# Kernel tuning notes

Hardware: AMD Instinct MI355X
Metric: run time of the kernel (lower is better)

## Reference

```python
import jax, jax.numpy as jnp
import numpy as np

# ASPPConv constants (from init_kwargs)
K = 9                      # kernel_size
DILATION = 6
PAD = DILATION * (K // 2)  # 24, 'same' padding for dilated conv
SIGMA = DILATION * 1.0     # self.sigma = dilation * sigma
BN_EPS = 1e-5


def setup_inputs() -> dict:
    key = jax.random.key(0)
    k1, k2, k3 = jax.random.split(key, 3)
    B, C, O, L = 8, 256, 16384, 0  # placeholder to keep names readable
    B, Cin, Cout, L = 8, 256, 256, 16384
    x = jax.random.normal(k1, (B, Cin, L), dtype=jnp.float32)
    coords = jax.random.uniform(k2, (B, 3, L), dtype=jnp.float32)  # xyz per point
    weight = jax.random.normal(k3, (Cout, Cin, K), dtype=jnp.float32) * 0.05
    gamma = jnp.ones((Cout,), jnp.float32)
    beta = jnp.zeros((Cout,), jnp.float32)
    return {"x": x, "coords": coords, "weight": weight, "gamma": gamma, "beta": beta}


def _weighted_conv1d(x, coords, weight):
    """Dilated conv1d where each tap is scaled by a Gaussian of the squared
    euclidean distance between the tap's coordinates and the center point's
    coordinates: w_k = exp(-||c_k - c_center||^2 / (2*sigma^2)).
    Zero padding (matches F.unfold) for both x and coords."""
    B, C, L = x.shape
    x_pad = jnp.pad(x, ((0, 0), (0, 0), (PAD, PAD)))
    c_pad = jnp.pad(coords, ((0, 0), (0, 0), (PAD, PAD)))
    inv_2s2 = 1.0 / (2.0 * SIGMA * SIGMA)
    out = jnp.zeros((B, weight.shape[0], L), x.dtype)
    # K=9 taps: small fixed loop; avoids materializing the [B,C,K,L] unfold.
    for k in range(K):
        off = k * DILATION
        xk = jax.lax.dynamic_slice_in_dim(x_pad, off, L, axis=2)   # [B,C,L]
        ck = jax.lax.dynamic_slice_in_dim(c_pad, off, L, axis=2)   # [B,3,L]
        dist2 = jnp.sum((ck - coords) ** 2, axis=1)                # [B,L]
        wk = jnp.exp(-dist2 * inv_2s2)                             # [B,L]
        out = out + jnp.einsum('bcl,oc->bol', xk * wk[:, None, :], weight[:, :, k])
    return out


def reference(x, coords, weight, gamma, beta):
    y = _weighted_conv1d(x, coords, weight)                        # [B,O,L]
    # BatchNorm1d (training mode): stats over batch and length per channel
    mean = jnp.mean(y, axis=(0, 2), keepdims=True)
    var = jnp.var(y, axis=(0, 2), keepdims=True)
    y = (y - mean) * jax.lax.rsqrt(var + BN_EPS)
    y = y * gamma[None, :, None] + beta[None, :, None]
    return jax.nn.relu(y)
```

## Files before the change

### kernel.cpp

```cpp
#include <hip/hip_runtime.h>
#include <hip/hip_bf16.h>

#define LEN   16384
#define CIN   256
#define COUT  256
#define NB    8
#define NTAP  9
#define DIL   6
#define PADW  24
#define NSTEP 72
#define PADROWS (LEN + 2*PADW)

typedef __bf16 bf16x8 __attribute__((ext_vector_type(8)));
typedef float  f32x4  __attribute__((ext_vector_type(4)));
typedef unsigned short u16;
typedef u16 u16x8 __attribute__((ext_vector_type(8)));

#define WKT_BYTES  (NB*NTAP*LEN*4)
#define WB_BYTES   (NSTEP*256*32*2)
#define XT_OFF     (WKT_BYTES + WB_BYTES)
#define XT_BYTES   ((size_t)NB*PADROWS*256*2)
#define SUMS_OFF   (XT_OFF + XT_BYTES)
#define SCB_OFF    (SUMS_OFF + 512*4)

#define GLOAD_LDS(g, l) __builtin_amdgcn_global_load_lds( \
    (const __attribute__((address_space(1))) void*)(g),   \
    (__attribute__((address_space(3))) void*)(l), 16, 0, 0)

__device__ __forceinline__ u16 f2bf(float v) {
    unsigned u = __builtin_bit_cast(unsigned, v);
    u += 0x7FFFu + ((u >> 16) & 1u);
    return (u16)(u >> 16);
}

__global__ __launch_bounds__(256) void k_wk(const float* __restrict__ coords,
                                            float* __restrict__ wkt) {
    int i = blockIdx.x * 256 + threadIdx.x;
    if (i >= NB * NTAP * LEN) return;
    int l = i & (LEN - 1);
    int bk = i >> 14;
    int k = bk % NTAP, b = bk / NTAP;
    const float* cb = coords + (size_t)b * 3 * LEN;
    int lt = l + k * DIL - PADW;
    bool ok = (unsigned)lt < (unsigned)LEN;
    float d2 = 0.f;
#pragma unroll
    for (int j = 0; j < 3; ++j) {
        float cc = cb[j * LEN + l];
        float ct = ok ? cb[j * LEN + lt] : 0.f;
        float d = ct - cc;
        d2 += d * d;
    }
    wkt[i] = expf(-d2 * (1.f / 72.f));
}

__global__ __launch_bounds__(256) void k_wb(const float* __restrict__ W,
                                            u16* __restrict__ Wb) {
    int i = blockIdx.x * 256 + threadIdx.x;
    if (i >= NSTEP * 256 * 32) return;
    int j = i & 31;
    int o = (i >> 5) & 255;
    int s = i >> 13;
    int tap   = s % 9;
    int chunk = s / 9;
    int c = chunk * 32 + j;
    Wb[i] = f2bf(W[((size_t)o * CIN + c) * NTAP + tap]);
}

__global__ __launch_bounds__(256) void k_xt(const float* __restrict__ x,
                                            u16* __restrict__ xt) {
    __shared__ float t[64 * 65];
    const int tid = threadIdx.x;
    const int cg  = blockIdx.x;
    const int rg  = blockIdx.y;
    const int b   = blockIdx.z;
    const int lx0 = rg * 64 - PADW;
#pragma unroll
    for (int i = 0; i < 4; ++i) {
        int c  = i * 16 + (tid >> 4);
        int l4 = (tid & 15) * 4;
        int lx = lx0 + l4;
        f32x4 v = {};
        if (lx >= 0 && lx + 3 < LEN)
            v = *reinterpret_cast<const f32x4*>(
                x + ((size_t)b * CIN + cg * 64 + c) * LEN + lx);
        float* tr = &t[c * 65 + l4];
        tr[0] = v[0]; tr[1] = v[1]; tr[2] = v[2]; tr[3] = v[3];
    }
    __syncthreads();
#pragma unroll
    for (int m = 0; m < 2; ++m) {
        int l    = m * 32 + (tid >> 3);
        int c0   = (tid & 7) * 8;
        int prow = rg * 64 + l;
        if (prow < PADROWS) {
            u16x8 o;
#pragma unroll
            for (int j = 0; j < 8; ++j) o[j] = f2bf(t[(c0 + j) * 65 + l]);
            *reinterpret_cast<u16x8*>(
                xt + ((size_t)b * PADROWS + prow) * 256 + cg * 64 + c0) = o;
        }
    }
}

__global__ __launch_bounds__(256, 3) void k_conv(
    const u16*   __restrict__ xt,
    const float* __restrict__ wkt,
    const u16*   __restrict__ Wb,
    float* __restrict__ y,
    float* __restrict__ sums)
{
    const int lt = blockIdx.x;
    const int ob = blockIdx.y;
    const int b  = blockIdx.z;
    const int l0 = lt * 128;
    const int tid  = threadIdx.x;
    const int lane = tid & 63;
    const int wid  = tid >> 6;
    const int wr = wid >> 1;
    const int wc = wid & 1;

    __shared__ u16 As[3][4096];
    __shared__ u16 Bs[3][4096];
    __shared__ float wkl[NTAP * 128];

    for (int i = tid; i < NTAP * 128; i += 256) {
        int k = i >> 7, l = i & 127;
        wkl[i] = wkt[((size_t)b * NTAP + k) * LEN + l0 + l];
    }

    f32x4 acc[4][4] = {};

    const u16* wbBase = Wb + (size_t)ob * 4096;
    const u16* xtBase = xt + (size_t)b * PADROWS * 256;
    const int srcswz = ((lane & 3) ^ ((lane >> 3) & 3)) * 8;
    const int rsub   = lane >> 2;

    auto stage = [&](int slot, int tap, int chunk) {
        const int s = chunk * 9 + tap;
#pragma unroll
        for (int j = 0; j < 2; ++j) {
            const int q = wid * 2 + j;
            const u16* ga = wbBase + (size_t)s * 8192 + (q * 16 + rsub) * 32 + srcswz;
            GLOAD_LDS(ga, &As[slot][q * 512]);
            const u16* gb = xtBase
                + (size_t)(l0 + q * 16 + rsub + 6 * tap) * 256
                + chunk * 32 + srcswz;
            GLOAD_LDS(gb, &Bs[slot][q * 512]);
        }
    };

    const int fr    = lane & 15;
    const int rdoff = fr * 32 + (((lane >> 4) ^ ((fr >> 1) & 3)) * 8);
    const int col   = lane & 15;
    const int rg    = lane >> 4;

    stage(0, 0, 0);
    stage(1, 1, 0);

    int rslot = 0, wslot = 2;
    int tap = 0, chunk = 0;
    int st = 2, sc = 0;
    const f32x4 zf = {};

    for (int s = 0; s < NSTEP; ++s) {
        if (s < NSTEP - 1) asm volatile("s_waitcnt vmcnt(4) lgkmcnt(0)" ::: "memory");
        else               asm volatile("s_waitcnt vmcnt(0) lgkmcnt(0)" ::: "memory");
        asm volatile("s_barrier" ::: "memory");
        if (s + 2 < NSTEP) {
            stage(wslot, st, sc);
            if (++st == NTAP) { st = 0; ++sc; }
        }

        bf16x8 afr[4], bfr[4];
        const u16* Ab = &As[rslot][wr * 2048 + rdoff];
        const u16* Bb = &Bs[rslot][wc * 2048 + rdoff];
#pragma unroll
        for (int mi = 0; mi < 4; ++mi)
            afr[mi] = *reinterpret_cast<const bf16x8*>(Ab + mi * 512);
#pragma unroll
        for (int ni = 0; ni < 4; ++ni)
            bfr[ni] = *reinterpret_cast<const bf16x8*>(Bb + ni * 512);

        float wv[4];
#pragma unroll
        for (int ni = 0; ni < 4; ++ni)
            wv[ni] = wkl[tap * 128 + wc * 64 + ni * 16 + col];

        __builtin_amdgcn_s_setprio(1);
#pragma unroll
        for (int mi = 0; mi < 4; ++mi) {
            f32x4 t0 = __builtin_amdgcn_mfma_f32_16x16x32_bf16(afr[mi], bfr[0], zf, 0, 0, 0);
            f32x4 t1 = __builtin_amdgcn_mfma_f32_16x16x32_bf16(afr[mi], bfr[1], zf, 0, 0, 0);
            f32x4 t2 = __builtin_amdgcn_mfma_f32_16x16x32_bf16(afr[mi], bfr[2], zf, 0, 0, 0);
            f32x4 t3 = __builtin_amdgcn_mfma_f32_16x16x32_bf16(afr[mi], bfr[3], zf, 0, 0, 0);
#pragma unroll
            for (int r = 0; r < 4; ++r) {
                acc[mi][0][r] += wv[0] * t0[r];
                acc[mi][1][r] += wv[1] * t1[r];
                acc[mi][2][r] += wv[2] * t2[r];
                acc[mi][3][r] += wv[3] * t3[r];
            }
        }
        __builtin_amdgcn_s_setprio(0);

        if (++tap == NTAP) { tap = 0; ++chunk; }
        rslot = (rslot == 2) ? 0 : rslot + 1;
        wslot = (wslot == 2) ? 0 : wslot + 1;
    }

    float* yb = y + ((size_t)b * COUT + ob * 128 + wr * 64) * LEN + l0 + wc * 64;
#pragma unroll
    for (int mi = 0; mi < 4; ++mi) {
#pragma unroll
        for (int r = 0; r < 4; ++r) {
            const int o_loc = mi * 16 + rg * 4 + r;
            float s1 = 0.f, s2 = 0.f;
#pragma unroll
            for (int ni = 0; ni < 4; ++ni) {
                float v = acc[mi][ni][r];
                yb[(size_t)o_loc * LEN + ni * 16 + col] = v;
                s1 += v;
                s2 += v * v;
            }
#pragma unroll
            for (int m = 1; m < 16; m <<= 1) {
                s1 += __shfl_xor(s1, m, 64);
                s2 += __shfl_xor(s2, m, 64);
            }
            if (col == 0) {
                int o = ob * 128 + wr * 64 + o_loc;
                atomicAdd(&sums[o], s1);
                atomicAdd(&sums[COUT + o], s2);
            }
        }
    }
}

__global__ __launch_bounds__(256) void k_stats(const float* __restrict__ sums,
                                               const float* __restrict__ gamma,
                                               const float* __restrict__ beta,
                                               float* __restrict__ scb) {
    int o = threadIdx.x;
    const float inv_n = 1.f / (float)(NB * LEN);
    float mean = sums[o] * inv_n;
    float var  = sums[COUT + o] * inv_n - mean * mean;
    float sc = gamma[o] * rsqrtf(var + 1e-5f);
    scb[o]        = sc;
    scb[COUT + o] = beta[o] - mean * sc;
}

__global__ __launch_bounds__(256) void k_norm(float* __restrict__ y,
                                              const float* __restrict__ scb) {
    const int total4 = NB * COUT * LEN / 4;
    int i = blockIdx.x * 256 + threadIdx.x;
    for (; i < total4; i += gridDim.x * 256) {
        f32x4 v = reinterpret_cast<f32x4*>(y)[i];
        int o = (i >> 12) & 255;
        float sc = scb[o], bi = scb[COUT + o];
#pragma unroll
        for (int j = 0; j < 4; ++j)
            v[j] = fmaxf(v[j] * sc + bi, 0.f);
        reinterpret_cast<f32x4*>(y)[i] = v;
    }
}

extern "C" void kernel_launch(void* const* d_in, const int* in_sizes, int n_in,
                              void* d_out, int out_size, void* d_ws, size_t ws_size,
                              hipStream_t stream) {
    const float* x      = (const float*)d_in[0];
    const float* coords = (const float*)d_in[1];
    const float* W      = (const float*)d_in[2];
    const float* gamma  = (const float*)d_in[3];
    const float* beta   = (const float*)d_in[4];
    float* out = (float*)d_out;
    char*  ws  = (char*)d_ws;

    float* wkt  = (float*)ws;
    u16*   Wb   = (u16*)(ws + WKT_BYTES);
    u16*   xtp  = (u16*)(ws + XT_OFF);
    float* sums = (float*)(ws + SUMS_OFF);
    float* scb  = (float*)(ws + SCB_OFF);

    hipMemsetAsync(sums, 0, 512 * 4, stream);

    k_wk<<<(NB * NTAP * LEN + 255) / 256, 256, 0, stream>>>(coords, wkt);
    k_wb<<<(NSTEP * 256 * 32 + 255) / 256, 256, 0, stream>>>(W, Wb);
    k_xt<<<dim3(4, (PADROWS + 63) / 64, NB), 256, 0, stream>>>(x, xtp);

    dim3 g(LEN / 128, 2, NB);
    k_conv<<<g, 256, 0, stream>>>(xtp, wkt, Wb, out, sums);

    k_stats<<<1, 256, 0, stream>>>(sums, gamma, beta, scb);
    k_norm<<<2048, 256, 0, stream>>>(out, scb);
}
```

Baseline: 449.9 us.

## Fold Gaussian tap weights into B tile via register staging, accumulate MFMA directly

```diff
diff --git a/kernel.cpp b/kernel.cpp
--- a/kernel.cpp
+++ b/kernel.cpp
@@ -122,93 +122,122 @@
 
     __shared__ u16 As[3][4096];
     __shared__ u16 Bs[3][4096];
-    __shared__ float wkl[NTAP * 128];
-
-    for (int i = tid; i < NTAP * 128; i += 256) {
-        int k = i >> 7, l = i & 127;
-        wkl[i] = wkt[((size_t)b * NTAP + k) * LEN + l0 + l];
-    }
 
     f32x4 acc[4][4] = {};
 
-    const u16* wbBase = Wb + (size_t)ob * 4096;
-    const u16* xtBase = xt + (size_t)b * PADROWS * 256;
+    const u16*   wbBase = Wb + (size_t)ob * 4096;
+    const u16*   xtBase = xt + (size_t)b * PADROWS * 256;
+    const float* wkBase = wkt + (size_t)b * NTAP * LEN;
+
     const int srcswz = ((lane & 3) ^ ((lane >> 3) & 3)) * 8;
     const int rsub   = lane >> 2;
-
-    auto stage = [&](int slot, int tap, int chunk) {
-        const int s = chunk * 9 + tap;
+    auto stageA = [&](int slot, int s) {
 #pragma unroll
         for (int j = 0; j < 2; ++j) {
             const int q = wid * 2 + j;
-            const u16* ga = wbBase + (size_t)s * 8192 + (q * 16 + rsub) * 32 + srcswz;
-            GLOAD_LDS(ga, &As[slot][q * 512]);
-            const u16* gb = xtBase
-                + (size_t)(l0 + q * 16 + rsub + 6 * tap) * 256
-                + chunk * 32 + srcswz;
-            GLOAD_LDS(gb, &Bs[slot][q * 512]);
+            GLOAD_LDS(wbBase + (size_t)s * 8192 + (q * 16 + rsub) * 32 + srcswz,
+                      &As[slot][q * 512]);
         }
     };
 
+    const int brow = tid >> 1;
+    const int bh   = tid & 1;
+    const int bsw  = (brow >> 1) & 3;
+    const int bwr  = brow * 32 + (((bh * 2) ^ bsw) * 8);
+
+    auto gloadB = [&](u16x8& v0, u16x8& v1, float& w, int tap, int chunk) {
+        const u16* gp = xtBase + (size_t)(l0 + brow + 6 * tap) * 256
+                        + chunk * 32 + bh * 16;
+        v0 = *reinterpret_cast<const u16x8*>(gp);
+        v1 = *reinterpret_cast<const u16x8*>(gp + 8);
+        w  = wkBase[(size_t)tap * LEN + l0 + brow];
+    };
+    auto writeB = [&](int slot, u16x8 v0, u16x8 v1, float w) {
+        u16x8 o0, o1;
+#pragma unroll
+        for (int j = 0; j < 8; ++j) {
+            float f0 = __builtin_bit_cast(float, ((unsigned)v0[j]) << 16) * w;
+            float f1 = __builtin_bit_cast(float, ((unsigned)v1[j]) << 16) * w;
+            o0[j] = f2bf(f0);
+            o1[j] = f2bf(f1);
+        }
+        *reinterpret_cast<u16x8*>(&Bs[slot][bwr])     = o0;
+        *reinterpret_cast<u16x8*>(&Bs[slot][bwr ^ 8]) = o1;
+    };
+
     const int fr    = lane & 15;
-    const int rdoff = fr * 32 + (((lane >> 4) ^ ((fr >> 1) & 3)) * 8);
-    const int col   = lane & 15;
-    const int rg    = lane >> 4;
-
-    stage(0, 0, 0);
-    stage(1, 1, 0);
-
-    int rslot = 0, wslot = 2;
-    int tap = 0, chunk = 0;
-    int st = 2, sc = 0;
-    const f32x4 zf = {};
-
-    for (int s = 0; s < NSTEP; ++s) {
-        if (s < NSTEP - 1) asm volatile("s_waitcnt vmcnt(4) lgkmcnt(0)" ::: "memory");
-        else               asm volatile("s_waitcnt vmcnt(0) lgkmcnt(0)" ::: "memory");
-        asm volatile("s_barrier" ::: "memory");
-        if (s + 2 < NSTEP) {
-            stage(wslot, st, sc);
-            if (++st == NTAP) { st = 0; ++sc; }
-        }
-
-        bf16x8 afr[4], bfr[4];
-        const u16* Ab = &As[rslot][wr * 2048 + rdoff];
-        const u16* Bb = &Bs[rslot][wc * 2048 + rdoff];
+    const int kg    = lane >> 4;
+    const int rdoff = fr * 32 + ((kg ^ ((fr >> 1) & 3)) * 8);
+    bf16x8 afr[4], bfr[4];
+    auto readFrags = [&](int slot) {
+        const u16* Ab = &As[slot][wr * 2048 + rdoff];
+        const u16* Bb = &Bs[slot][wc * 2048 + rdoff];
 #pragma unroll
         for (int mi = 0; mi < 4; ++mi)
             afr[mi] = *reinterpret_cast<const bf16x8*>(Ab + mi * 512);
 #pragma unroll
         for (int ni = 0; ni < 4; ++ni)
             bfr[ni] = *reinterpret_cast<const bf16x8*>(Bb + ni * 512);
-
-        float wv[4];
-#pragma unroll
-        for (int ni = 0; ni < 4; ++ni)
-            wv[ni] = wkl[tap * 128 + wc * 64 + ni * 16 + col];
-
+    };
+    auto domfma = [&]() {
         __builtin_amdgcn_s_setprio(1);
 #pragma unroll
-        for (int mi = 0; mi < 4; ++mi) {
-            f32x4 t0 = __builtin_amdgcn_mfma_f32_16x16x32_bf16(afr[mi], bfr[0], zf, 0, 0, 0);
-            f32x4 t1 = __builtin_amdgcn_mfma_f32_16x16x32_bf16(afr[mi], bfr[1], zf, 0, 0, 0);
-            f32x4 t2 = __builtin_amdgcn_mfma_f32_16x16x32_bf16(afr[mi], bfr[2], zf, 0, 0, 0);
-            f32x4 t3 = __builtin_amdgcn_mfma_f32_16x16x32_bf16(afr[mi], bfr[3], zf, 0, 0, 0);
-#pragma unroll
-            for (int r = 0; r < 4; ++r) {
-                acc[mi][0][r] += wv[0] * t0[r];
-                acc[mi][1][r] += wv[1] * t1[r];
-                acc[mi][2][r] += wv[2] * t2[r];
-                acc[mi][3][r] += wv[3] * t3[r];
-            }
-        }
+        for (int mi = 0; mi < 4; ++mi)
+#pragma unroll
+            for (int ni = 0; ni < 4; ++ni)
+                acc[mi][ni] = __builtin_amdgcn_mfma_f32_16x16x32_bf16(
+                    afr[mi], bfr[ni], acc[mi][ni], 0, 0, 0);
         __builtin_amdgcn_s_setprio(0);
-
-        if (++tap == NTAP) { tap = 0; ++chunk; }
-        rslot = (rslot == 2) ? 0 : rslot + 1;
-        wslot = (wslot == 2) ? 0 : wslot + 1;
-    }
-
+    };
+
+    u16x8 vE0, vE1, vO0, vO1;
+    float wE, wO;
+    stageA(0, 0);
+    gloadB(vE0, vE1, wE, 0, 0);
+    __builtin_amdgcn_sched_barrier(0);
+    stageA(1, 1);
+    gloadB(vO0, vO1, wO, 1, 0);
+    asm volatile("s_waitcnt vmcnt(5)" ::: "memory");
+    writeB(0, vE0, vE1, wE);
+    asm volatile("s_waitcnt lgkmcnt(0)" ::: "memory");
+    asm volatile("s_barrier" ::: "memory");
+
+    int sl0 = 0, sl1 = 1, sl2 = 2;
+    int st = 2, sc = 0;
+
+    for (int t = 0; t < 35; ++t) {
+        stageA(sl2, 2 * t + 2);
+        gloadB(vE0, vE1, wE, st, sc);
+        if (++st == NTAP) { st = 0; ++sc; }
+        readFrags(sl0);
+        asm volatile("s_waitcnt vmcnt(5)" ::: "memory");
+        writeB(sl1, vO0, vO1, wO);
+        asm volatile("s_waitcnt lgkmcnt(0)" ::: "memory");
+        asm volatile("s_barrier" ::: "memory");
+        domfma();
+        stageA(sl0, 2 * t + 3);
+        gloadB(vO0, vO1, wO, st, sc);
+        if (++st == NTAP) { st = 0; ++sc; }
+        readFrags(sl1);
+        asm volatile("s_waitcnt vmcnt(5)" ::: "memory");
+        writeB(sl2, vE0, vE1, wE);
+        asm volatile("s_waitcnt lgkmcnt(0)" ::: "memory");
+        asm volatile("s_barrier" ::: "memory");
+        domfma();
+        int tmp = sl2; sl2 = sl1; sl1 = sl0; sl0 = tmp;
+    }
+
+    readFrags(sl0);
+    asm volatile("s_waitcnt vmcnt(0)" ::: "memory");
+    writeB(sl1, vO0, vO1, wO);
+    asm volatile("s_waitcnt lgkmcnt(0)" ::: "memory");
+    asm volatile("s_barrier" ::: "memory");
+    domfma();
+    readFrags(sl1);
+    domfma();
+
+    const int col = lane & 15;
+    const int rg  = lane >> 4;
     float* yb = y + ((size_t)b * COUT + ob * 128 + wr * 64) * LEN + l0 + wc * 64;
 #pragma unroll
     for (int mi = 0; mi < 4; ++mi) {
```

Result: faster. 426.0 us (-5.3%).

## Switch conv GEMM to fp16 and fold tap weights into B operand

Applied to the files above, without the earlier changes.

```diff
diff --git a/kernel.cpp b/kernel.cpp
--- a/kernel.cpp
+++ b/kernel.cpp
@@ -11,7 +11,7 @@
 #define NSTEP 72
 #define PADROWS (LEN + 2*PADW)
 
-typedef __bf16 bf16x8 __attribute__((ext_vector_type(8)));
+typedef _Float16 f16x8 __attribute__((ext_vector_type(8)));
 typedef float  f32x4  __attribute__((ext_vector_type(4)));
 typedef unsigned short u16;
 typedef u16 u16x8 __attribute__((ext_vector_type(8)));
@@ -27,10 +27,9 @@
     (const __attribute__((address_space(1))) void*)(g),   \
     (__attribute__((address_space(3))) void*)(l), 16, 0, 0)
 
-__device__ __forceinline__ u16 f2bf(float v) {
-    unsigned u = __builtin_bit_cast(unsigned, v);
-    u += 0x7FFFu + ((u >> 16) & 1u);
-    return (u16)(u >> 16);
+__device__ __forceinline__ u16 f2h(float v) {
+    _Float16 h = (_Float16)v;
+    return __builtin_bit_cast(u16, h);
 }
 
 __global__ __launch_bounds__(256) void k_wk(const float* __restrict__ coords,
@@ -64,7 +63,7 @@
     int tap   = s % 9;
     int chunk = s / 9;
     int c = chunk * 32 + j;
-    Wb[i] = f2bf(W[((size_t)o * CIN + c) * NTAP + tap]);
+    Wb[i] = f2h(W[((size_t)o * CIN + c) * NTAP + tap]);
 }
 
 __global__ __launch_bounds__(256) void k_xt(const float* __restrict__ x,
@@ -96,7 +95,7 @@
         if (prow < PADROWS) {
             u16x8 o;
 #pragma unroll
-            for (int j = 0; j < 8; ++j) o[j] = f2bf(t[(c0 + j) * 65 + l]);
+            for (int j = 0; j < 8; ++j) o[j] = f2h(t[(c0 + j) * 65 + l]);
             *reinterpret_cast<u16x8*>(
                 xt + ((size_t)b * PADROWS + prow) * 256 + cg * 64 + c0) = o;
         }
@@ -122,11 +121,11 @@
 
     __shared__ u16 As[3][4096];
     __shared__ u16 Bs[3][4096];
-    __shared__ float wkl[NTAP * 128];
+    __shared__ _Float16 wkl16[NTAP * 128];
 
     for (int i = tid; i < NTAP * 128; i += 256) {
         int k = i >> 7, l = i & 127;
-        wkl[i] = wkt[((size_t)b * NTAP + k) * LEN + l0 + l];
+        wkl16[i] = (_Float16)wkt[((size_t)b * NTAP + k) * LEN + l0 + l];
     }
 
     f32x4 acc[4][4] = {};
@@ -161,7 +160,6 @@
     int rslot = 0, wslot = 2;
     int tap = 0, chunk = 0;
     int st = 2, sc = 0;
-    const f32x4 zf = {};
 
     for (int s = 0; s < NSTEP; ++s) {
         if (s < NSTEP - 1) asm volatile("s_waitcnt vmcnt(4) lgkmcnt(0)" ::: "memory");
@@ -172,36 +170,29 @@
             if (++st == NTAP) { st = 0; ++sc; }
         }
 
-        bf16x8 afr[4], bfr[4];
+        f16x8 afr[4], bs[4];
         const u16* Ab = &As[rslot][wr * 2048 + rdoff];
         const u16* Bb = &Bs[rslot][wc * 2048 + rdoff];
 #pragma unroll
         for (int mi = 0; mi < 4; ++mi)
-            afr[mi] = *reinterpret_cast<const bf16x8*>(Ab + mi * 512);
-#pragma unroll
-        for (int ni = 0; ni < 4; ++ni)
-            bfr[ni] = *reinterpret_cast<const bf16x8*>(Bb + ni * 512);
-
-        float wv[4];
-#pragma unroll
-        for (int ni = 0; ni < 4; ++ni)
-            wv[ni] = wkl[tap * 128 + wc * 64 + ni * 16 + col];
+            afr[mi] = *reinterpret_cast<const f16x8*>(Ab + mi * 512);
+#pragma unroll
+        for (int ni = 0; ni < 4; ++ni) {
+            f16x8 bf = *reinterpret_cast<const f16x8*>(Bb + ni * 512);
+            _Float16 w = wkl16[tap * 128 + wc * 64 + ni * 16 + col];
+            f16x8 w8;
+#pragma unroll
+            for (int j = 0; j < 8; ++j) w8[j] = w;
+            bs[ni] = bf * w8;
+        }
 
         __builtin_amdgcn_s_setprio(1);
 #pragma unroll
-        for (int mi = 0; mi < 4; ++mi) {
-            f32x4 t0 = __builtin_amdgcn_mfma_f32_16x16x32_bf16(afr[mi], bfr[0], zf, 0, 0, 0);
-            f32x4 t1 = __builtin_amdgcn_mfma_f32_16x16x32_bf16(afr[mi], bfr[1], zf, 0, 0, 0);
-            f32x4 t2 = __builtin_amdgcn_mfma_f32_16x16x32_bf16(afr[mi], bfr[2], zf, 0, 0, 0);
-            f32x4 t3 = __builtin_amdgcn_mfma_f32_16x16x32_bf16(afr[mi], bfr[3], zf, 0, 0, 0);
-#pragma unroll
-            for (int r = 0; r < 4; ++r) {
-                acc[mi][0][r] += wv[0] * t0[r];
-                acc[mi][1][r] += wv[1] * t1[r];
-                acc[mi][2][r] += wv[2] * t2[r];
-                acc[mi][3][r] += wv[3] * t3[r];
-            }
-        }
+        for (int mi = 0; mi < 4; ++mi)
+#pragma unroll
+            for (int ni = 0; ni < 4; ++ni)
+                acc[mi][ni] = __builtin_amdgcn_mfma_f32_16x16x32_f16(
+                    afr[mi], bs[ni], acc[mi][ni], 0, 0, 0);
         __builtin_amdgcn_s_setprio(0);
 
         if (++tap == NTAP) { tap = 0; ++chunk; }
```

Measured after the change: 420.7 us. 1.07x faster.
